# Performance work log

Hardware: AMD Instinct MI355X
Metric: run time of the kernel (lower is better)

The kernel has to match this reference:

```python
import jax, jax.numpy as jnp
import numpy as np
import math

N_HEADS = 8
D_EMBED = 512
D_CROSS = 768
FF_DIM = 2048
D_HEAD = D_EMBED // N_HEADS


def _gelu_tanh(x):
    # matches the module's hand-written tanh GELU
    return 0.5 * x * (1.0 + jnp.tanh(jnp.sqrt(2.0 / jnp.pi) * (x + 0.044715 * x ** 3)))


def _layer_norm(x, g, b, eps=1e-5):
    mu = jnp.mean(x, axis=-1, keepdims=True)
    var = jnp.var(x, axis=-1, keepdims=True)
    return (x - mu) * jax.lax.rsqrt(var + eps) * g + b


def setup_inputs() -> dict:
    key = jax.random.key(0)
    ks = jax.random.split(key, 20)
    s = 0.02
    inp = {
        "x": jax.random.normal(ks[0], (2, 4096, D_EMBED), jnp.float32),
        "y": jax.random.normal(ks[1], (2, 77, D_CROSS), jnp.float32),
        # self-attention: fused in_proj [D, 3D]
        "sa_in_w": jax.random.normal(ks[2], (D_EMBED, 3 * D_EMBED), jnp.float32) * s,
        "sa_in_b": jnp.zeros((3 * D_EMBED,), jnp.float32),
        "sa_out_w": jax.random.normal(ks[3], (D_EMBED, D_EMBED), jnp.float32) * s,
        "sa_out_b": jnp.zeros((D_EMBED,), jnp.float32),
        # cross-attention
        "ca_q_w": jax.random.normal(ks[4], (D_EMBED, D_EMBED), jnp.float32) * s,
        "ca_q_b": jnp.zeros((D_EMBED,), jnp.float32),
        "ca_k_w": jax.random.normal(ks[5], (D_CROSS, D_EMBED), jnp.float32) * s,
        "ca_k_b": jnp.zeros((D_EMBED,), jnp.float32),
        "ca_v_w": jax.random.normal(ks[6], (D_CROSS, D_EMBED), jnp.float32) * s,
        "ca_v_b": jnp.zeros((D_EMBED,), jnp.float32),
        "ca_out_w": jax.random.normal(ks[7], (D_EMBED, D_EMBED), jnp.float32) * s,
        "ca_out_b": jnp.zeros((D_EMBED,), jnp.float32),
        # feed-forward
        "ff_w1": jax.random.normal(ks[8], (D_EMBED, FF_DIM), jnp.float32) * s,
        "ff_b1": jnp.zeros((FF_DIM,), jnp.float32),
        "ff_w2": jax.random.normal(ks[9], (FF_DIM, D_EMBED), jnp.float32) * s,
        "ff_b2": jnp.zeros((D_EMBED,), jnp.float32),
        # layer norms
        "ln1_g": jnp.ones((D_EMBED,), jnp.float32),
        "ln1_b": jnp.zeros((D_EMBED,), jnp.float32),
        "ln2_g": jnp.ones((D_EMBED,), jnp.float32),
        "ln2_b": jnp.zeros((D_EMBED,), jnp.float32),
        "ln3_g": jnp.ones((D_EMBED,), jnp.float32),
        "ln3_b": jnp.zeros((D_EMBED,), jnp.float32),
    }
    return inp


def _mha(q, k, v):
    # q,k,v: [B, S, D] -> split heads -> attention -> merge
    B, Sq, D = q.shape
    Skv = k.shape[1]
    qh = q.reshape(B, Sq, N_HEADS, D_HEAD).transpose(0, 2, 1, 3)
    kh = k.reshape(B, Skv, N_HEADS, D_HEAD).transpose(0, 2, 1, 3)
    vh = v.reshape(B, Skv, N_HEADS, D_HEAD).transpose(0, 2, 1, 3)
    scores = jnp.einsum("bhqd,bhkd->bhqk", qh, kh) / math.sqrt(D_HEAD)
    w = jax.nn.softmax(scores, axis=-1)
    out = jnp.einsum("bhqk,bhkd->bhqd", w, vh)
    return out.transpose(0, 2, 1, 3).reshape(B, Sq, D)


def reference(x, y, sa_in_w, sa_in_b, sa_out_w, sa_out_b,
              ca_q_w, ca_q_b, ca_k_w, ca_k_b, ca_v_w, ca_v_b, ca_out_w, ca_out_b,
              ff_w1, ff_b1, ff_w2, ff_b2,
              ln1_g, ln1_b, ln2_g, ln2_b, ln3_g, ln3_b):
    # self-attention (no causal mask; default causal_mask=False)
    qkv = x @ sa_in_w + sa_in_b
    q, k, v = jnp.split(qkv, 3, axis=-1)
    sa = _mha(q, k, v) @ sa_out_w + sa_out_b
    x = _layer_norm(x + sa, ln1_g, ln1_b)

    # cross-attention to y
    qc = x @ ca_q_w + ca_q_b
    kc = y @ ca_k_w + ca_k_b
    vc = y @ ca_v_w + ca_v_b
    ca = _mha(qc, kc, vc) @ ca_out_w + ca_out_b
    x = _layer_norm(x + ca, ln2_g, ln2_b)

    # feed-forward with tanh GELU
    ff = _gelu_tanh(x @ ff_w1 + ff_b1) @ ff_w2 + ff_b2
    x = _layer_norm(x + ff, ln3_g, ln3_b)
    return x
```

## Files before the change

### kernel.cpp

```cpp
#include <hip/hip_runtime.h>
#include <stdint.h>

typedef float floatx4 __attribute__((ext_vector_type(4)));
typedef __bf16 bf16x8 __attribute__((ext_vector_type(8)));
typedef unsigned int uintx4 __attribute__((ext_vector_type(4)));
typedef unsigned short ushort_t;

__device__ __forceinline__ float b2f(ushort_t u) {
  union { unsigned int i; float f; } x; x.i = ((unsigned int)u) << 16; return x.f;
}
__device__ __forceinline__ ushort_t f2b(float f) {
  union { float f; unsigned int i; } x; x.f = f;
  unsigned int i = x.i;
  return (ushort_t)((i + 0x7FFFu + ((i >> 16) & 1u)) >> 16);
}
__device__ __forceinline__ unsigned fbits(float f) {
  union { float f; unsigned u; } x; x.f = f; return x.u;
}
__device__ __forceinline__ unsigned pk_rne(float a, float b) {
#if __has_builtin(__builtin_amdgcn_cvt_pk_bf16_f32)
  return __builtin_bit_cast(unsigned, __builtin_amdgcn_cvt_pk_bf16_f32(a, b));
#else
  return (unsigned)f2b(a) | ((unsigned)f2b(b) << 16);
#endif
}
__device__ __forceinline__ unsigned pk_fast(float a, float b) {
#if __has_builtin(__builtin_amdgcn_cvt_pk_bf16_f32)
  return __builtin_bit_cast(unsigned, __builtin_amdgcn_cvt_pk_bf16_f32(a, b));
#else
  return (fbits(b) & 0xFFFF0000u) | (fbits(a) >> 16);
#endif
}
__device__ __forceinline__ uintx4 ld16(const void* p) {
  uintx4 v; __builtin_memcpy(&v, p, 16); return v;
}
__device__ __forceinline__ void st16(void* p, uintx4 v) { __builtin_memcpy(p, &v, 16); }
__device__ __forceinline__ floatx4 f4splat(float x) { floatx4 v = {x, x, x, x}; return v; }
__device__ __forceinline__ void sched_fence() { asm volatile("" ::: "memory"); }

__device__ __forceinline__ floatx4 mfma16(uintx4 a, uintx4 b, floatx4 c) {
  return __builtin_amdgcn_mfma_f32_16x16x32_bf16(
      __builtin_bit_cast(bf16x8, a), __builtin_bit_cast(bf16x8, b), c, 0, 0, 0);
}

__device__ __forceinline__ void gll16(const ushort_t* g, ushort_t* l) {
  __builtin_amdgcn_global_load_lds(
      (__attribute__((address_space(1))) void*)(g),
      (__attribute__((address_space(3))) void*)(l), 16, 0, 0);
}

template <int EPI, int NT>
__global__ __launch_bounds__(256, 2) void gemm_bt(
    const ushort_t* __restrict__ A, const ushort_t* __restrict__ Bt,
    const float* __restrict__ bias, ushort_t* __restrict__ Cout,
    int N, int K) {
  constexpr int NI = NT / 32;
  __shared__ alignas(16) ushort_t lA[128 * 32];
  __shared__ alignas(16) ushort_t lB[NT * 32];
  const int tid = threadIdx.x;
  const int wave = tid >> 6, lane = tid & 63;
  const int quad = lane >> 4, l16 = lane & 15;
  const int bm = blockIdx.y * 128, bn = blockIdx.x * NT;
  const int wm = (wave >> 1) * 64, wn = (wave & 1) * (NT / 2);

  const ushort_t* ag0 = A + (size_t)(bm + wave * 32 + (lane >> 2)) * K + (lane & 3) * 8;
  const ushort_t* ag1 = ag0 + (size_t)16 * K;
  ushort_t* la = lA + wave * 1024;
  const ushort_t* bg0;
  const ushort_t* bg1 = nullptr;
  ushort_t* lb;
  if (NT == 128) {
    bg0 = Bt + (size_t)(bn + wave * 32 + (lane >> 2)) * K + (lane & 3) * 8;
    bg1 = bg0 + (size_t)16 * K;
    lb = lB + wave * 1024;
  } else {
    bg0 = Bt + (size_t)(bn + wave * 16 + (lane >> 2)) * K + (lane & 3) * 8;
    lb = lB + wave * 512;
  }

  floatx4 acc[4][NI];
#pragma unroll
  for (int i = 0; i < 4; i++)
#pragma unroll
    for (int j = 0; j < NI; j++) acc[i][j] = f4splat(0.f);

  for (int k0 = 0; k0 < K; k0 += 32) {
    __syncthreads();
    gll16(ag0 + k0, la);
    gll16(ag1 + k0, la + 512);
    gll16(bg0 + k0, lb);
    if (NT == 128) gll16(bg1 + k0, lb + 512);
    __syncthreads();
    uintx4 af[4], bf[NI];
#pragma unroll
    for (int i = 0; i < 4; i++) af[i] = ld16(&lA[(wm + i * 16 + l16) * 32 + quad * 8]);
#pragma unroll
    for (int i = 0; i < NI; i++) bf[i] = ld16(&lB[(wn + i * 16 + l16) * 32 + quad * 8]);
#pragma unroll
    for (int mi = 0; mi < 4; mi++)
#pragma unroll
      for (int ni = 0; ni < NI; ni++) acc[mi][ni] = mfma16(af[mi], bf[ni], acc[mi][ni]);
  }

  float bv[NI];
#pragma unroll
  for (int ni = 0; ni < NI; ni++) bv[ni] = bias[bn + wn + ni * 16 + l16];

#pragma unroll
  for (int mi = 0; mi < 4; mi++)
#pragma unroll
    for (int ni = 0; ni < NI; ni++)
#pragma unroll
      for (int r = 0; r < 4; r++) {
        int row = bm + wm + mi * 16 + quad * 4 + r;
        int col = bn + wn + ni * 16 + l16;
        float v = acc[mi][ni][r] + bv[ni];
        if (EPI == 2) {
          float w = v + 0.044715f * v * v * v;
          float e = __builtin_amdgcn_exp2f(-2.3022084f * w);
          v = v * __builtin_amdgcn_rcpf(1.f + e);
        }
        Cout[(size_t)row * N + col] = f2b(v);
      }
}

struct TransJob { const float* in; ushort_t* out; int ldi, ldo, nbx, start; };
struct TransJobs8 { TransJob j[8]; };

__global__ __launch_bounds__(256) void prep(TransJobs8 jobs, const float* __restrict__ x,
                                            ushort_t* __restrict__ xbf,
                                            const float* __restrict__ y,
                                            ushort_t* __restrict__ ybf) {
  __shared__ float t[32][33];
  int bid = blockIdx.x;
  if (bid >= 8448) {
    int i = ((bid - 8448) * 256 + threadIdx.x) * 4;
    const int limit = 154 * 768;
    float v4[4];
    if (i + 4 <= limit) {
      __builtin_memcpy(v4, y + i, 16);
    } else {
#pragma unroll
      for (int j = 0; j < 4; j++) v4[j] = (i + j < limit) ? y[i + j] : 0.f;
    }
    unsigned o[2] = {pk_rne(v4[0], v4[1]), pk_rne(v4[2], v4[3])};
    __builtin_memcpy(ybf + i, o, 8);
    return;
  }
  if (bid >= 4352) {
    int i = ((bid - 4352) * 256 + threadIdx.x) * 4;
    float4 v; __builtin_memcpy(&v, x + i, 16);
    unsigned o[2] = {pk_rne(v.x, v.y), pk_rne(v.z, v.w)};
    __builtin_memcpy(xbf + i, o, 8);
    return;
  }
  int ji = 0;
#pragma unroll
  for (int i = 1; i < 8; i++)
    if (bid >= jobs.j[i].start) ji = i;
  TransJob J = jobs.j[ji];
  int local = bid - J.start;
  int by = local / J.nbx, bx = local - by * J.nbx;
  int r0 = by * 32, c0 = bx * 32;
  int tx = threadIdx.x & 31, ty = threadIdx.x >> 5;
#pragma unroll
  for (int i = 0; i < 4; i++)
    t[ty + 8 * i][tx] = J.in[(size_t)(r0 + ty + 8 * i) * J.ldi + c0 + tx];
  __syncthreads();
#pragma unroll
  for (int i = 0; i < 4; i++)
    J.out[(size_t)(c0 + ty + 8 * i) * J.ldo + r0 + tx] = f2b(t[tx][ty + 8 * i]);
}

__global__ __launch_bounds__(256) void pack(
    const ushort_t* __restrict__ qkv, ushort_t* __restrict__ KP,
    ushort_t* __restrict__ VP) {
  __shared__ ushort_t t[64 * 72];
  int bid = blockIdx.x;
  int tid = threadIdx.x;
  if (bid < 2048) {
    int g = bid * 256 + tid;
    int lane = g & 63;
    int frag = (g >> 6) & 7;
    int kt = (g >> 9) & 63;
    int bh = g >> 15;
    int b = bh >> 3, h = bh & 7;
    int ni = frag >> 1, kf = frag & 1;
    int l16 = lane & 15, quad = lane >> 4;
    const ushort_t* src = qkv + (size_t)(b * 4096 + kt * 64 + ni * 16 + l16) * 1536 +
                          512 + h * 64 + kf * 32 + quad * 8;
    st16(KP + (size_t)g * 8, ld16(src));
  } else {
    int local = bid - 2048;
    int bh = local >> 6, kt = local & 63;
    int b = bh >> 3, h = bh & 7;
#pragma unroll
    for (int i = 0; i < 2; i++) {
      int c = i * 256 + tid;
      int row = c >> 3, c8 = (c & 7) * 8;
      uintx4 d4 = ld16(qkv + (size_t)(b * 4096 + kt * 64 + row) * 1536 + 1024 + h * 64 + c8);
      ushort_t tmp[8];
      __builtin_memcpy(tmp, &d4, 16);
#pragma unroll
      for (int j = 0; j < 8; j++) t[(c8 + j) * 72 + row] = tmp[j];
    }
    __syncthreads();
#pragma unroll
    for (int i = 0; i < 2; i++) {
      int c = i * 256 + tid;
      int frag = c >> 6, lane = c & 63;
      int f = frag >> 2, dn = frag & 3;
      int l16 = lane & 15, quad = lane >> 4;
      uintx4 d4 = ld16(&t[(dn * 16 + l16) * 72 + f * 32 + quad * 8]);
      st16(VP + ((size_t)(bh * 64 + kt) * 8 + frag) * 512 + (size_t)lane * 8, d4);
    }
  }
}

__global__ __launch_bounds__(256, 2) void flash_self(
    const ushort_t* __restrict__ qkv, const ushort_t* __restrict__ KP,
    const ushort_t* __restrict__ VP, ushort_t* __restrict__ outp) {
  __shared__ alignas(16) ushort_t lPT[4 * 32 * 72];
  const int tid = threadIdx.x, wave = tid >> 6, lane = tid & 63;
  const int quad = lane >> 4, l16 = lane & 15;
  const int bh = blockIdx.x, b = bh >> 3, h = bh & 7;
  const int qt = blockIdx.y;

  const ushort_t* Qb = qkv + (size_t)b * 4096 * 1536 + h * 64;
  const ushort_t* KPb = KP + (size_t)bh * 64 * 4096;
  const ushort_t* VPb = VP + (size_t)bh * 64 * 4096;

  uintx4 qf[2][2];
#pragma unroll
  for (int mi = 0; mi < 2; mi++)
#pragma unroll
    for (int kf = 0; kf < 2; kf++)
      qf[mi][kf] = ld16(Qb + (size_t)(qt * 128 + wave * 32 + mi * 16 + l16) * 1536 +
                        kf * 32 + quad * 8);

  floatx4 O[2][4];
#pragma unroll
  for (int mi = 0; mi < 2; mi++)
#pragma unroll
    for (int dn = 0; dn < 4; dn++) O[mi][dn] = f4splat(0.f);
  float lsum[2] = {0.f, 0.f};
  const float c = 0.18033688f;
  ushort_t* PTw = lPT + wave * 32 * 72;

#pragma unroll 2
  for (int kt = 0; kt < 64; kt++) {
    const ushort_t* kb = KPb + kt * 4096;
    uintx4 kfr[4][2];
#pragma unroll
    for (int ni = 0; ni < 4; ni++)
#pragma unroll
      for (int kf = 0; kf < 2; kf++)
        kfr[ni][kf] = ld16(kb + ((ni * 2 + kf) * 64 + lane) * 8);

    floatx4 S[2][4];
#pragma unroll
    for (int ni = 0; ni < 4; ni++)
#pragma unroll
      for (int mi = 0; mi < 2; mi++) {
        floatx4 z = f4splat(0.f);
        z = mfma16(kfr[ni][0], qf[mi][0], z);
        z = mfma16(kfr[ni][1], qf[mi][1], z);
        S[mi][ni] = z;
      }

    const ushort_t* vbp = VPb + kt * 4096;
    uintx4 vf[2][4];
#pragma unroll
    for (int f = 0; f < 2; f++)
#pragma unroll
      for (int dn = 0; dn < 4; dn++)
        vf[f][dn] = ld16(vbp + ((f * 4 + dn) * 64 + lane) * 8);

#pragma unroll
    for (int mi = 0; mi < 2; mi++) {
      float rs = 0.f;
#pragma unroll
      for (int ni = 0; ni < 4; ni++) {
        float p0 = __builtin_amdgcn_exp2f(S[mi][ni][0] * c);
        float p1 = __builtin_amdgcn_exp2f(S[mi][ni][1] * c);
        float p2 = __builtin_amdgcn_exp2f(S[mi][ni][2] * c);
        float p3 = __builtin_amdgcn_exp2f(S[mi][ni][3] * c);
        rs += (p0 + p1) + (p2 + p3);
        unsigned dd[2] = {pk_fast(p0, p1), pk_fast(p2, p3)};
        __builtin_memcpy(&PTw[(mi * 16 + l16) * 72 + ni * 16 + quad * 4], dd, 8);
      }
      lsum[mi] += rs;
    }
    sched_fence();

#pragma unroll
    for (int f = 0; f < 2; f++) {
      uintx4 pf0 = ld16(&PTw[(0 + l16) * 72 + f * 32 + quad * 8]);
      uintx4 pf1 = ld16(&PTw[(16 + l16) * 72 + f * 32 + quad * 8]);
#pragma unroll
      for (int dn = 0; dn < 4; dn++) {
        O[0][dn] = mfma16(vf[f][dn], pf0, O[0][dn]);
        O[1][dn] = mfma16(vf[f][dn], pf1, O[1][dn]);
      }
    }
  }

#pragma unroll
  for (int mi = 0; mi < 2; mi++) {
    lsum[mi] += __shfl_xor(lsum[mi], 16);
    lsum[mi] += __shfl_xor(lsum[mi], 32);
  }

#pragma unroll
  for (int mi = 0; mi < 2; mi++) {
    float inv = 1.0f / lsum[mi];
    const size_t rowg = (size_t)b * 4096 + qt * 128 + wave * 32 + mi * 16 + l16;
#pragma unroll
    for (int dn = 0; dn < 4; dn++) {
      unsigned uu[2] = {pk_rne(O[mi][dn][0] * inv, O[mi][dn][1] * inv),
                        pk_rne(O[mi][dn][2] * inv, O[mi][dn][3] * inv)};
      __builtin_memcpy(outp + rowg * 512 + h * 64 + dn * 16 + quad * 4, uu, 8);
    }
  }
}

__global__ __launch_bounds__(256, 2) void cross_attn(
    const ushort_t* __restrict__ qc, const ushort_t* __restrict__ kc,
    const ushort_t* __restrict__ vc, ushort_t* __restrict__ outp) {
  __shared__ alignas(16) ushort_t lK[96 * 72];
  __shared__ alignas(16) ushort_t lV[64 * 104];
  __shared__ alignas(16) ushort_t lP[128 * 104];
  const int tid = threadIdx.x, wave = tid >> 6, lane = tid & 63;
  const int quad = lane >> 4, l16 = lane & 15;
  const int bh = blockIdx.y, b = bh >> 3, h = bh & 7;
  const int qt = blockIdx.x;

#pragma unroll
  for (int i = 0; i < 3; i++) {
    int ch = i * 256 + tid;
    int r = ch >> 3, c8 = ch & 7;
    uintx4 d = {0u, 0u, 0u, 0u};
    if (r < 77) d = ld16(kc + (size_t)(b * 77 + r) * 512 + h * 64 + c8 * 8);
    st16(&lK[r * 72 + c8 * 8], d);
  }
  for (int i = 0; i < 24; i++) {
    int e = i * 256 + tid;
    int dd = e / 96, s = e - dd * 96;
    ushort_t v = 0;
    if (s < 77) v = vc[(size_t)(b * 77 + s) * 512 + h * 64 + dd];
    lV[dd * 104 + s] = v;
  }
  __syncthreads();

  const int qr0 = qt * 128 + wave * 32;
  uintx4 qf[2][2];
#pragma unroll
  for (int mi = 0; mi < 2; mi++)
#pragma unroll
    for (int kf = 0; kf < 2; kf++)
      qf[mi][kf] =
          ld16(qc + (size_t)(b * 4096 + qr0 + mi * 16 + l16) * 512 + h * 64 + kf * 32 + quad * 8);

  floatx4 S[2][6];
#pragma unroll
  for (int ni = 0; ni < 6; ni++) {
    uintx4 k0 = ld16(&lK[(ni * 16 + l16) * 72 + quad * 8]);
    uintx4 k1 = ld16(&lK[(ni * 16 + l16) * 72 + 32 + quad * 8]);
#pragma unroll
    for (int mi = 0; mi < 2; mi++) {
      floatx4 z = f4splat(0.f);
      z = mfma16(qf[mi][0], k0, z);
      z = mfma16(qf[mi][1], k1, z);
      S[mi][ni] = z;
    }
  }
  const float c = 0.18033688f;
#pragma unroll
  for (int ni = 4; ni < 6; ni++)
    if (ni * 16 + l16 >= 77) {
      S[0][ni] = f4splat(-1e30f);
      S[1][ni] = f4splat(-1e30f);
    }

  floatx4 linv[2];
#pragma unroll
  for (int mi = 0; mi < 2; mi++) {
    floatx4 cm = S[mi][0];
#pragma unroll
    for (int ni = 1; ni < 6; ni++)
#pragma unroll
      for (int r = 0; r < 4; r++) cm[r] = fmaxf(cm[r], S[mi][ni][r]);
#pragma unroll
    for (int off = 1; off < 16; off <<= 1)
#pragma unroll
      for (int r = 0; r < 4; r++) cm[r] = fmaxf(cm[r], __shfl_xor(cm[r], off));
    floatx4 rs = f4splat(0.f);
#pragma unroll
    for (int ni = 0; ni < 6; ni++)
#pragma unroll
      for (int r = 0; r < 4; r++) {
        float p = __builtin_amdgcn_exp2f(S[mi][ni][r] * c - cm[r] * c);
        S[mi][ni][r] = p;
        rs[r] += p;
      }
#pragma unroll
    for (int off = 1; off < 16; off <<= 1)
#pragma unroll
      for (int r = 0; r < 4; r++) rs[r] += __shfl_xor(rs[r], off);
#pragma unroll
    for (int r = 0; r < 4; r++) linv[mi][r] = 1.0f / rs[r];
#pragma unroll
    for (int ni = 0; ni < 6; ni++)
#pragma unroll
      for (int r = 0; r < 4; r++)
        lP[(wave * 32 + mi * 16 + quad * 4 + r) * 104 + ni * 16 + l16] = f2b(S[mi][ni][r]);
  }
  sched_fence();

  floatx4 O[2][4];
#pragma unroll
  for (int mi = 0; mi < 2; mi++)
#pragma unroll
    for (int dn = 0; dn < 4; dn++) O[mi][dn] = f4splat(0.f);
#pragma unroll
  for (int kf = 0; kf < 3; kf++) {
    uintx4 pa0 = ld16(&lP[(wave * 32 + 0 + l16) * 104 + kf * 32 + quad * 8]);
    uintx4 pa1 = ld16(&lP[(wave * 32 + 16 + l16) * 104 + kf * 32 + quad * 8]);
#pragma unroll
    for (int dn = 0; dn < 4; dn++) {
      uintx4 vb = ld16(&lV[(dn * 16 + l16) * 104 + kf * 32 + quad * 8]);
      O[0][dn] = mfma16(pa0, vb, O[0][dn]);
      O[1][dn] = mfma16(pa1, vb, O[1][dn]);
    }
  }
#pragma unroll
  for (int mi = 0; mi < 2; mi++)
#pragma unroll
    for (int dn = 0; dn < 4; dn++)
#pragma unroll
      for (int r = 0; r < 4; r++) {
        int row = b * 4096 + qt * 128 + wave * 32 + mi * 16 + quad * 4 + r;
        int col = h * 64 + dn * 16 + l16;
        outp[(size_t)row * 512 + col] = f2b(O[mi][dn][r] * linv[mi][r]);
      }
}

template <int RESF>
__global__ __launch_bounds__(256) void ln_kernel(
    const ushort_t* __restrict__ p, const void* __restrict__ resv,
    const float* __restrict__ g, const float* __restrict__ bb,
    float* __restrict__ out32, ushort_t* __restrict__ outbf) {
  const int row = blockIdx.x * 4 + (threadIdx.x >> 6);
  const int lane = threadIdx.x & 63;
  const size_t base = (size_t)row * 512;
  float v[8];
  float s = 0.f, ss = 0.f;
#pragma unroll
  for (int i = 0; i < 2; i++) {
    int cidx = i * 256 + lane * 4;
    ushort_t pb[4];
    __builtin_memcpy(pb, p + base + cidx, 8);
    float rv[4];
    if (RESF) {
      __builtin_memcpy(rv, (const float*)resv + base + cidx, 16);
    } else {
      ushort_t rr[4];
      __builtin_memcpy(rr, (const ushort_t*)resv + base + cidx, 8);
#pragma unroll
      for (int j = 0; j < 4; j++) rv[j] = b2f(rr[j]);
    }
#pragma unroll
    for (int j = 0; j < 4; j++) {
      float a = b2f(pb[j]) + rv[j];
      v[i * 4 + j] = a;
      s += a;
      ss += a * a;
    }
  }
#pragma unroll
  for (int off = 1; off < 64; off <<= 1) {
    s += __shfl_xor(s, off);
    ss += __shfl_xor(ss, off);
  }
  float mean = s * (1.f / 512.f);
  float var = ss * (1.f / 512.f) - mean * mean;
  float rstd = rsqrtf(var + 1e-5f);
#pragma unroll
  for (int i = 0; i < 2; i++) {
    int cidx = i * 256 + lane * 4;
    float gv[4], bv2[4];
    __builtin_memcpy(gv, g + cidx, 16);
    __builtin_memcpy(bv2, bb + cidx, 16);
    float y[4];
#pragma unroll
    for (int j = 0; j < 4; j++) y[j] = (v[i * 4 + j] - mean) * rstd * gv[j] + bv2[j];
    if (out32) __builtin_memcpy(out32 + base + cidx, y, 16);
    if (outbf) {
      unsigned o[2] = {pk_rne(y[0], y[1]), pk_rne(y[2], y[3])};
      __builtin_memcpy(outbf + base + cidx, o, 8);
    }
  }
}

extern "C" void kernel_launch(void* const* d_in, const int* in_sizes, int n_in,
                              void* d_out, int out_size, void* d_ws, size_t ws_size,
                              hipStream_t stream) {
  const size_t MiB = 1048576;
  if (ws_size < 64 * MiB) return;

  const float* x        = (const float*)d_in[0];
  const float* y        = (const float*)d_in[1];
  const float* sa_in_w  = (const float*)d_in[2];
  const float* sa_in_b  = (const float*)d_in[3];
  const float* sa_out_w = (const float*)d_in[4];
  const float* sa_out_b = (const float*)d_in[5];
  const float* ca_q_w   = (const float*)d_in[6];
  const float* ca_q_b   = (const float*)d_in[7];
  const float* ca_k_w   = (const float*)d_in[8];
  const float* ca_k_b   = (const float*)d_in[9];
  const float* ca_v_w   = (const float*)d_in[10];
  const float* ca_v_b   = (const float*)d_in[11];
  const float* ca_out_w = (const float*)d_in[12];
  const float* ca_out_b = (const float*)d_in[13];
  const float* ff_w1    = (const float*)d_in[14];
  const float* ff_b1    = (const float*)d_in[15];
  const float* ff_w2    = (const float*)d_in[16];
  const float* ff_b2    = (const float*)d_in[17];
  const float* ln1_g    = (const float*)d_in[18];
  const float* ln1_b    = (const float*)d_in[19];
  const float* ln2_g    = (const float*)d_in[20];
  const float* ln2_b    = (const float*)d_in[21];
  const float* ln3_g    = (const float*)d_in[22];
  const float* ln3_b    = (const float*)d_in[23];

  char* w = (char*)d_ws;
  ushort_t* QKV  = (ushort_t*)(w + 0);
  ushort_t* QC   = (ushort_t*)(w + 0);
  ushort_t* FF   = (ushort_t*)(w + 0);
  ushort_t* YBF  = (ushort_t*)(w + 24 * MiB);
  ushort_t* WTk  = (ushort_t*)(w + 24 * MiB + 524288);
  ushort_t* WTv  = (ushort_t*)(w + 24 * MiB + 1572864);
  ushort_t* ATT  = (ushort_t*)(w + 24 * MiB);
  ushort_t* XBF  = (ushort_t*)(w + 32 * MiB);
  ushort_t* KP   = (ushort_t*)(w + 32 * MiB);
  ushort_t* XB0b = (ushort_t*)(w + 32 * MiB);
  ushort_t* VP   = (ushort_t*)(w + 40 * MiB);
  ushort_t* XB1b = (ushort_t*)(w + 40 * MiB);
  ushort_t* P    = (ushort_t*)(w + 48 * MiB);
  ushort_t* WT   = (ushort_t*)(w + 56 * MiB);
  ushort_t* KC   = (ushort_t*)(w + 63 * MiB);
  ushort_t* VC   = KC + 256 * 512;

  ushort_t* WT_sain  = WT;
  ushort_t* WT_saout = WT_sain + 786432;
  ushort_t* WT_caq   = WT_saout + 262144;
  ushort_t* WT_caout = WT_caq + 262144;
  ushort_t* WT_ff1   = WT_caout + 262144;
  ushort_t* WT_ff2   = WT_ff1 + 1048576;

  TransJobs8 tj;
  tj.j[0] = TransJob{sa_in_w,  WT_sain,  1536, 512, 48, 0};
  tj.j[1] = TransJob{sa_out_w, WT_saout, 512,  512, 16, 768};
  tj.j[2] = TransJob{ca_q_w,   WT_caq,   512,  512, 16, 1024};
  tj.j[3] = TransJob{ca_out_w, WT_caout, 512,  512, 16, 1280};
  tj.j[4] = TransJob{ff_w1,    WT_ff1,   2048, 512, 64, 1536};
  tj.j[5] = TransJob{ff_w2,    WT_ff2,   512, 2048, 16, 2560};
  tj.j[6] = TransJob{ca_k_w,   WTk,      512,  768, 16, 3584};
  tj.j[7] = TransJob{ca_v_w,   WTv,      512,  768, 16, 3968};
  prep<<<8640, 256, 0, stream>>>(tj, x, XBF, y, YBF);

  gemm_bt<0, 64><<<dim3(8, 2), 256, 0, stream>>>(YBF, WTk, ca_k_b, KC, 512, 768);
  gemm_bt<0, 64><<<dim3(8, 2), 256, 0, stream>>>(YBF, WTv, ca_v_b, VC, 512, 768);

  gemm_bt<0, 128><<<dim3(12, 64), 256, 0, stream>>>(XBF, WT_sain, sa_in_b, QKV, 1536, 512);
  pack<<<3072, 256, 0, stream>>>(QKV, KP, VP);
  flash_self<<<dim3(16, 32), 256, 0, stream>>>(QKV, KP, VP, ATT);
  gemm_bt<0, 64><<<dim3(8, 64), 256, 0, stream>>>(ATT, WT_saout, sa_out_b, P, 512, 512);
  ln_kernel<1><<<2048, 256, 0, stream>>>(P, x, ln1_g, ln1_b, nullptr, XB0b);

  gemm_bt<0, 64><<<dim3(8, 64), 256, 0, stream>>>(XB0b, WT_caq, ca_q_b, QC, 512, 512);
  cross_attn<<<dim3(32, 16), 256, 0, stream>>>(QC, KC, VC, ATT);
  gemm_bt<0, 64><<<dim3(8, 64), 256, 0, stream>>>(ATT, WT_caout, ca_out_b, P, 512, 512);
  ln_kernel<0><<<2048, 256, 0, stream>>>(P, XB0b, ln2_g, ln2_b, nullptr, XB1b);

  gemm_bt<2, 128><<<dim3(16, 64), 256, 0, stream>>>(XB1b, WT_ff1, ff_b1, FF, 2048, 512);
  gemm_bt<0, 64><<<dim3(8, 64), 256, 0, stream>>>(FF, WT_ff2, ff_b2, P, 512, 2048);
  ln_kernel<0><<<2048, 256, 0, stream>>>(P, XB1b, ln3_g, ln3_b, (float*)d_out, nullptr);
}
```

Before: 396.9 us.

## Shrink flash_self query tile, raise occupancy bounds, merge cross K/V GEMMs

The self-attention kernel now processes 16 query rows per wave (64 per block) instead of 32, which halves the accumulator and score registers and the LDS footprint, and the grid doubles to 1024 blocks. Launch bounds are raised to 3 blocks per SM for flash_self and the 64-wide GEMMs, with the GEMM body split into a shared device function. The two small cross-attention K/V projections are merged into a single launch. The trade-off is that each K/V fragment loaded in flash_self is now reused by half as many query rows, which doubles K/V traffic, and the tighter register budget may cause spills.

Result: slower. 430.0 us (+8.3%).

```diff
diff --git a/kernel.cpp b/kernel.cpp
--- a/kernel.cpp
+++ b/kernel.cpp
@@ -50,17 +50,16 @@
 }
 
 template <int EPI, int NT>
-__global__ __launch_bounds__(256, 2) void gemm_bt(
+__device__ __forceinline__ void gemm_core(
     const ushort_t* __restrict__ A, const ushort_t* __restrict__ Bt,
     const float* __restrict__ bias, ushort_t* __restrict__ Cout,
-    int N, int K) {
+    int N, int K, int bm, int bn) {
   constexpr int NI = NT / 32;
   __shared__ alignas(16) ushort_t lA[128 * 32];
   __shared__ alignas(16) ushort_t lB[NT * 32];
   const int tid = threadIdx.x;
   const int wave = tid >> 6, lane = tid & 63;
   const int quad = lane >> 4, l16 = lane & 15;
-  const int bm = blockIdx.y * 128, bn = blockIdx.x * NT;
   const int wm = (wave >> 1) * 64, wn = (wave & 1) * (NT / 2);
 
   const ushort_t* ag0 = A + (size_t)(bm + wave * 32 + (lane >> 2)) * K + (lane & 3) * 8;
@@ -122,6 +121,32 @@
         }
         Cout[(size_t)row * N + col] = f2b(v);
       }
+}
+
+template <int EPI>
+__global__ __launch_bounds__(256, 2) void gemm_bt128(
+    const ushort_t* __restrict__ A, const ushort_t* __restrict__ Bt,
+    const float* __restrict__ bias, ushort_t* __restrict__ Cout, int N, int K) {
+  gemm_core<EPI, 128>(A, Bt, bias, Cout, N, K, blockIdx.y * 128, blockIdx.x * 128);
+}
+
+template <int EPI>
+__global__ __launch_bounds__(256, 3) void gemm_bt64(
+    const ushort_t* __restrict__ A, const ushort_t* __restrict__ Bt,
+    const float* __restrict__ bias, ushort_t* __restrict__ Cout, int N, int K) {
+  gemm_core<EPI, 64>(A, Bt, bias, Cout, N, K, blockIdx.y * 128, blockIdx.x * 64);
+}
+
+__global__ __launch_bounds__(256, 3) void gemm_ckv(
+    const ushort_t* __restrict__ YBF, const ushort_t* __restrict__ WTk,
+    const float* __restrict__ bk, ushort_t* __restrict__ KC,
+    const ushort_t* __restrict__ WTv, const float* __restrict__ bv,
+    ushort_t* __restrict__ VC) {
+  int by = blockIdx.y;
+  const ushort_t* Bt = (by < 2) ? WTk : WTv;
+  const float* bb = (by < 2) ? bk : bv;
+  ushort_t* O = (by < 2) ? KC : VC;
+  gemm_core<0, 64>(YBF, Bt, bb, O, 512, 768, (by & 1) * 128, blockIdx.x * 64);
 }
 
 struct TransJob { const float* in; ushort_t* out; int ldi, ldo, nbx, start; };
@@ -217,10 +242,10 @@
   }
 }
 
-__global__ __launch_bounds__(256, 2) void flash_self(
+__global__ __launch_bounds__(256, 3) void flash_self(
     const ushort_t* __restrict__ qkv, const ushort_t* __restrict__ KP,
     const ushort_t* __restrict__ VP, ushort_t* __restrict__ outp) {
-  __shared__ alignas(16) ushort_t lPT[4 * 32 * 72];
+  __shared__ alignas(16) ushort_t lPT[4 * 16 * 72];
   const int tid = threadIdx.x, wave = tid >> 6, lane = tid & 63;
   const int quad = lane >> 4, l16 = lane & 15;
   const int bh = blockIdx.x, b = bh >> 3, h = bh & 7;
@@ -230,22 +255,16 @@
   const ushort_t* KPb = KP + (size_t)bh * 64 * 4096;
   const ushort_t* VPb = VP + (size_t)bh * 64 * 4096;
 
-  uintx4 qf[2][2];
-#pragma unroll
-  for (int mi = 0; mi < 2; mi++)
-#pragma unroll
-    for (int kf = 0; kf < 2; kf++)
-      qf[mi][kf] = ld16(Qb + (size_t)(qt * 128 + wave * 32 + mi * 16 + l16) * 1536 +
-                        kf * 32 + quad * 8);
-
-  floatx4 O[2][4];
-#pragma unroll
-  for (int mi = 0; mi < 2; mi++)
-#pragma unroll
-    for (int dn = 0; dn < 4; dn++) O[mi][dn] = f4splat(0.f);
-  float lsum[2] = {0.f, 0.f};
+  const int qrow = qt * 64 + wave * 16 + l16;
+  uintx4 qf0 = ld16(Qb + (size_t)qrow * 1536 + quad * 8);
+  uintx4 qf1 = ld16(Qb + (size_t)qrow * 1536 + 32 + quad * 8);
+
+  floatx4 O[4];
+#pragma unroll
+  for (int dn = 0; dn < 4; dn++) O[dn] = f4splat(0.f);
+  float lsum = 0.f;
   const float c = 0.18033688f;
-  ushort_t* PTw = lPT + wave * 32 * 72;
+  ushort_t* PTw = lPT + wave * 16 * 72;
 
 #pragma unroll 2
   for (int kt = 0; kt < 64; kt++) {
@@ -257,16 +276,14 @@
       for (int kf = 0; kf < 2; kf++)
         kfr[ni][kf] = ld16(kb + ((ni * 2 + kf) * 64 + lane) * 8);
 
-    floatx4 S[2][4];
-#pragma unroll
-    for (int ni = 0; ni < 4; ni++)
-#pragma unroll
-      for (int mi = 0; mi < 2; mi++) {
-        floatx4 z = f4splat(0.f);
-        z = mfma16(kfr[ni][0], qf[mi][0], z);
-        z = mfma16(kfr[ni][1], qf[mi][1], z);
-        S[mi][ni] = z;
-      }
+    floatx4 S[4];
+#pragma unroll
+    for (int ni = 0; ni < 4; ni++) {
+      floatx4 z = f4splat(0.f);
+      z = mfma16(kfr[ni][0], qf0, z);
+      z = mfma16(kfr[ni][1], qf1, z);
+      S[ni] = z;
+    }
 
     const ushort_t* vbp = VPb + kt * 4096;
     uintx4 vf[2][4];
@@ -276,51 +293,38 @@
       for (int dn = 0; dn < 4; dn++)
         vf[f][dn] = ld16(vbp + ((f * 4 + dn) * 64 + lane) * 8);
 
-#pragma unroll
-    for (int mi = 0; mi < 2; mi++) {
-      float rs = 0.f;
-#pragma unroll
-      for (int ni = 0; ni < 4; ni++) {
-        float p0 = __builtin_amdgcn_exp2f(S[mi][ni][0] * c);
-        float p1 = __builtin_amdgcn_exp2f(S[mi][ni][1] * c);
-        float p2 = __builtin_amdgcn_exp2f(S[mi][ni][2] * c);
-        float p3 = __builtin_amdgcn_exp2f(S[mi][ni][3] * c);
-        rs += (p0 + p1) + (p2 + p3);
-        unsigned dd[2] = {pk_fast(p0, p1), pk_fast(p2, p3)};
-        __builtin_memcpy(&PTw[(mi * 16 + l16) * 72 + ni * 16 + quad * 4], dd, 8);
-      }
-      lsum[mi] += rs;
-    }
+    float rs = 0.f;
+#pragma unroll
+    for (int ni = 0; ni < 4; ni++) {
+      float p0 = __builtin_amdgcn_exp2f(S[ni][0] * c);
+      float p1 = __builtin_amdgcn_exp2f(S[ni][1] * c);
+      float p2 = __builtin_amdgcn_exp2f(S[ni][2] * c);
+      float p3 = __builtin_amdgcn_exp2f(S[ni][3] * c);
+      rs += (p0 + p1) + (p2 + p3);
+      unsigned dd[2] = {pk_fast(p0, p1), pk_fast(p2, p3)};
+      __builtin_memcpy(&PTw[l16 * 72 + ni * 16 + quad * 4], dd, 8);
+    }
+    lsum += rs;
     sched_fence();
 
 #pragma unroll
     for (int f = 0; f < 2; f++) {
-      uintx4 pf0 = ld16(&PTw[(0 + l16) * 72 + f * 32 + quad * 8]);
-      uintx4 pf1 = ld16(&PTw[(16 + l16) * 72 + f * 32 + quad * 8]);
-#pragma unroll
-      for (int dn = 0; dn < 4; dn++) {
-        O[0][dn] = mfma16(vf[f][dn], pf0, O[0][dn]);
-        O[1][dn] = mfma16(vf[f][dn], pf1, O[1][dn]);
-      }
-    }
-  }
-
-#pragma unroll
-  for (int mi = 0; mi < 2; mi++) {
-    lsum[mi] += __shfl_xor(lsum[mi], 16);
-    lsum[mi] += __shfl_xor(lsum[mi], 32);
-  }
-
-#pragma unroll
-  for (int mi = 0; mi < 2; mi++) {
-    float inv = 1.0f / lsum[mi];
-    const size_t rowg = (size_t)b * 4096 + qt * 128 + wave * 32 + mi * 16 + l16;
-#pragma unroll
-    for (int dn = 0; dn < 4; dn++) {
-      unsigned uu[2] = {pk_rne(O[mi][dn][0] * inv, O[mi][dn][1] * inv),
-                        pk_rne(O[mi][dn][2] * inv, O[mi][dn][3] * inv)};
-      __builtin_memcpy(outp + rowg * 512 + h * 64 + dn * 16 + quad * 4, uu, 8);
-    }
+      uintx4 pf = ld16(&PTw[l16 * 72 + f * 32 + quad * 8]);
+#pragma unroll
+      for (int dn = 0; dn < 4; dn++) O[dn] = mfma16(vf[f][dn], pf, O[dn]);
+    }
+  }
+
+  lsum += __shfl_xor(lsum, 16);
+  lsum += __shfl_xor(lsum, 32);
+
+  float inv = 1.0f / lsum;
+  const size_t rowg = (size_t)b * 4096 + qrow;
+#pragma unroll
+  for (int dn = 0; dn < 4; dn++) {
+    unsigned uu[2] = {pk_rne(O[dn][0] * inv, O[dn][1] * inv),
+                      pk_rne(O[dn][2] * inv, O[dn][3] * inv)};
+    __builtin_memcpy(outp + rowg * 512 + h * 64 + dn * 16 + quad * 4, uu, 8);
   }
 }
 
@@ -569,21 +573,20 @@
   tj.j[7] = TransJob{ca_v_w,   WTv,      512,  768, 16, 3968};
   prep<<<8640, 256, 0, stream>>>(tj, x, XBF, y, YBF);
 
-  gemm_bt<0, 64><<<dim3(8, 2), 256, 0, stream>>>(YBF, WTk, ca_k_b, KC, 512, 768);
-  gemm_bt<0, 64><<<dim3(8, 2), 256, 0, stream>>>(YBF, WTv, ca_v_b, VC, 512, 768);
-
-  gemm_bt<0, 128><<<dim3(12, 64), 256, 0, stream>>>(XBF, WT_sain, sa_in_b, QKV, 1536, 512);
+  gemm_ckv<<<dim3(8, 4), 256, 0, stream>>>(YBF, WTk, ca_k_b, KC, WTv, ca_v_b, VC);
+
+  gemm_bt128<0><<<dim3(12, 64), 256, 0, stream>>>(XBF, WT_sain, sa_in_b, QKV, 1536, 512);
   pack<<<3072, 256, 0, stream>>>(QKV, KP, VP);
-  flash_self<<<dim3(16, 32), 256, 0, stream>>>(QKV, KP, VP, ATT);
-  gemm_bt<0, 64><<<dim3(8, 64), 256, 0, stream>>>(ATT, WT_saout, sa_out_b, P, 512, 512);
+  flash_self<<<dim3(16, 64), 256, 0, stream>>>(QKV, KP, VP, ATT);
+  gemm_bt64<0><<<dim3(8, 64), 256, 0, stream>>>(ATT, WT_saout, sa_out_b, P, 512, 512);
   ln_kernel<1><<<2048, 256, 0, stream>>>(P, x, ln1_g, ln1_b, nullptr, XB0b);
 
-  gemm_bt<0, 64><<<dim3(8, 64), 256, 0, stream>>>(XB0b, WT_caq, ca_q_b, QC, 512, 512);
+  gemm_bt64<0><<<dim3(8, 64), 256, 0, stream>>>(XB0b, WT_caq, ca_q_b, QC, 512, 512);
   cross_attn<<<dim3(32, 16), 256, 0, stream>>>(QC, KC, VC, ATT);
-  gemm_bt<0, 64><<<dim3(8, 64), 256, 0, stream>>>(ATT, WT_caout, ca_out_b, P, 512, 512);
+  gemm_bt64<0><<<dim3(8, 64), 256, 0, stream>>>(ATT, WT_caout, ca_out_b, P, 512, 512);
   ln_kernel<0><<<2048, 256, 0, stream>>>(P, XB0b, ln2_g, ln2_b, nullptr, XB1b);
 
-  gemm_bt<2, 128><<<dim3(16, 64), 256, 0, stream>>>(XB1b, WT_ff1, ff_b1, FF, 2048, 512);
-  gemm_bt<0, 64><<<dim3(8, 64), 256, 0, stream>>>(FF, WT_ff2, ff_b2, P, 512, 2048);
+  gemm_bt128<2><<<dim3(16, 64), 256, 0, stream>>>(XB1b, WT_ff1, ff_b1, FF, 2048, 512);
+  gemm_bt64<0><<<dim3(8, 64), 256, 0, stream>>>(FF, WT_ff2, ff_b2, P, 512, 2048);
   ln_kernel<0><<<2048, 256, 0, stream>>>(P, XB1b, ln3_g, ln3_b, (float*)d_out, nullptr);
 }
```
